# Performance work log

Hardware: AMD Instinct MI355X
Metric: run time of the kernel (lower is better)

Reference implementation:

```python
import jax, jax.numpy as jnp
import numpy as np

N_NODES = 100000
N_EDGES = 1200000
D = 64


def setup_inputs() -> dict:
    key = jax.random.key(0)
    ks = jax.random.split(key, 11)
    feats = jax.random.normal(ks[0], (N_NODES, D), dtype=jnp.float32)
    src = jax.random.randint(ks[1], (N_EDGES,), 0, N_NODES)
    dst = jax.random.randint(ks[2], (N_EDGES,), 0, N_NODES)
    s = 0.1  # small init scale
    W1 = jax.random.normal(ks[3], (D, D), dtype=jnp.float32) * s
    b1 = jnp.zeros((D,), dtype=jnp.float32)
    Wr1 = jax.random.normal(ks[4], (D, D), dtype=jnp.float32) * s
    br1 = jnp.zeros((D,), dtype=jnp.float32)
    W2 = jax.random.normal(ks[5], (D, D), dtype=jnp.float32) * s
    b2 = jnp.zeros((D,), dtype=jnp.float32)
    Wr2 = jax.random.normal(ks[6], (D, D), dtype=jnp.float32) * s
    br2 = jnp.zeros((D,), dtype=jnp.float32)
    return {"feats": feats, "W1": W1, "b1": b1, "Wr1": Wr1, "br1": br1,
            "W2": W2, "b2": b2, "Wr2": Wr2, "br2": br2,
            "src": src, "dst": dst}


def _gcn_layer(x, W, b, Wr, br, src, dst):
    # dgl GraphConv(norm='none'): aggregate sum of transformed neighbor feats + bias, then ReLU
    xw = x @ W                                        # [N, D]
    agg = jax.ops.segment_sum(xw[src], dst, num_segments=x.shape[0])  # gather-scatter
    conv = jax.nn.relu(agg + b)
    # residual branch: activation(Linear(feats))
    res = jax.nn.relu(x @ Wr + br)
    return conv + res  # dropout=0.0, batchnorm=False


def reference(feats, W1, b1, Wr1, br1, W2, b2, Wr2, br2, src, dst):
    h = _gcn_layer(feats, W1, b1, Wr1, br1, src, dst)
    h = _gcn_layer(h, W2, b2, Wr2, br2, src, dst)
    return h
```

## Files before the change

### kernel.cpp

```cpp
#include <hip/hip_runtime.h>

#define D 64
#define NBMAX 256
#define BCHUNK 4096
#define CAP 8192
#define CAP_PACK 12288

typedef unsigned short ushort_t;
typedef __attribute__((ext_vector_type(8))) short bf16x8;
typedef __attribute__((ext_vector_type(4))) float floatx4;

static __device__ __forceinline__ ushort_t f2bf(float x) {
  unsigned u = __float_as_uint(x);
  unsigned r = (u + 0x7FFF + ((u >> 16) & 1)) >> 16;
  return (ushort_t)r;
}
static __device__ __forceinline__ float bf2f(ushort_t u) {
  return __uint_as_float(((unsigned)u) << 16);
}

__global__ __launch_bounds__(256) void gemm_res_mfma_kernel(
    const float* __restrict__ x, const float* __restrict__ W,
    const float* __restrict__ Wr, const float* __restrict__ br,
    ushort_t* __restrict__ xw, ushort_t* __restrict__ res, int n_nodes,
    int* __restrict__ gtail, int* __restrict__ off_tail, int n_edges) {
  if (blockIdx.x == 0) {
    if (threadIdx.x < NBMAX) gtail[threadIdx.x] = (int)threadIdx.x * CAP_PACK;
    if (threadIdx.x == 0) *off_tail = n_edges;
  }
  const int lane = threadIdx.x & 63;
  const int wid = threadIdx.x >> 6;
  const int sub = lane & 15;
  const int q = lane >> 4;

  bf16x8 bW[4][2], bR[4][2];
#pragma unroll
  for (int t = 0; t < 4; ++t) {
#pragma unroll
    for (int s = 0; s < 2; ++s) {
      bf16x8 fw, fr;
#pragma unroll
      for (int j = 0; j < 8; ++j) {
        const int k = s * 32 + q * 8 + j;
        const int c = t * 16 + sub;
        fw[j] = (short)f2bf(W[k * D + c]);
        fr[j] = (short)f2bf(Wr[k * D + c]);
      }
      bW[t][s] = fw;
      bR[t][s] = fr;
    }
  }
  float brv[4];
#pragma unroll
  for (int t = 0; t < 4; ++t) brv[t] = br[t * 16 + sub];

  const int n_tiles = (n_nodes + 15) >> 4;
  const int wave_id = blockIdx.x * 4 + wid;
  const int n_waves = gridDim.x * 4;
  for (int tile = wave_id; tile < n_tiles; tile += n_waves) {
    const int n0 = tile << 4;
    const bool full = (n0 + 16 <= n_nodes);
    bf16x8 a0h, a0l, a1h, a1l;
    float v[16];
    if (full) {
      const float* xp = x + (size_t)(n0 + sub) * D + q * 8;
      *(float4*)(v + 0)  = *(const float4*)(xp);
      *(float4*)(v + 4)  = *(const float4*)(xp + 4);
      *(float4*)(v + 8)  = *(const float4*)(xp + 32);
      *(float4*)(v + 12) = *(const float4*)(xp + 36);
    } else {
      const bool ok = (n0 + sub) < n_nodes;
      const float* xp = x + (size_t)(n0 + sub) * D + q * 8;
#pragma unroll
      for (int j = 0; j < 8; ++j) {
        v[j] = ok ? xp[j] : 0.f;
        v[8 + j] = ok ? xp[32 + j] : 0.f;
      }
    }
#pragma unroll
    for (int j = 0; j < 8; ++j) {
      const ushort_t h0 = f2bf(v[j]);
      a0h[j] = (short)h0;
      a0l[j] = (short)f2bf(v[j] - bf2f(h0));
      const ushort_t h1 = f2bf(v[8 + j]);
      a1h[j] = (short)h1;
      a1l[j] = (short)f2bf(v[8 + j] - bf2f(h1));
    }
    floatx4 accW[4], accR[4];
#pragma unroll
    for (int t = 0; t < 4; ++t) {
      accW[t] = (floatx4){0.f, 0.f, 0.f, 0.f};
      accR[t] = (floatx4){0.f, 0.f, 0.f, 0.f};
    }
#pragma unroll
    for (int t = 0; t < 4; ++t) {
      accW[t] = __builtin_amdgcn_mfma_f32_16x16x32_bf16(a0h, bW[t][0], accW[t], 0, 0, 0);
      accW[t] = __builtin_amdgcn_mfma_f32_16x16x32_bf16(a0l, bW[t][0], accW[t], 0, 0, 0);
      accW[t] = __builtin_amdgcn_mfma_f32_16x16x32_bf16(a1h, bW[t][1], accW[t], 0, 0, 0);
      accW[t] = __builtin_amdgcn_mfma_f32_16x16x32_bf16(a1l, bW[t][1], accW[t], 0, 0, 0);
      accR[t] = __builtin_amdgcn_mfma_f32_16x16x32_bf16(a0h, bR[t][0], accR[t], 0, 0, 0);
      accR[t] = __builtin_amdgcn_mfma_f32_16x16x32_bf16(a0l, bR[t][0], accR[t], 0, 0, 0);
      accR[t] = __builtin_amdgcn_mfma_f32_16x16x32_bf16(a1h, bR[t][1], accR[t], 0, 0, 0);
      accR[t] = __builtin_amdgcn_mfma_f32_16x16x32_bf16(a1l, bR[t][1], accR[t], 0, 0, 0);
    }
    if (full) {
#pragma unroll
      for (int t = 0; t < 4; ++t) {
#pragma unroll
        for (int i = 0; i < 4; ++i) {
          const size_t r = (size_t)(n0 + q * 4 + i) * D + t * 16 + sub;
          xw[r] = f2bf(accW[t][i]);
          res[r] = f2bf(fmaxf(accR[t][i] + brv[t], 0.f));
        }
      }
    } else {
#pragma unroll
      for (int t = 0; t < 4; ++t) {
#pragma unroll
        for (int i = 0; i < 4; ++i) {
          const int rr = n0 + q * 4 + i;
          if (rr < n_nodes) {
            const size_t r = (size_t)rr * D + t * 16 + sub;
            xw[r] = f2bf(accW[t][i]);
            res[r] = f2bf(fmaxf(accR[t][i] + brv[t], 0.f));
          }
        }
      }
    }
  }
}

__global__ __launch_bounds__(256) void binpack_kernel(
    const int* __restrict__ src, const int* __restrict__ dst,
    int* __restrict__ gtail, unsigned* __restrict__ packed, int n_edges) {
  __shared__ int start[NBMAX], cur[NBMAX], gpos[NBMAX];
  __shared__ unsigned sorted[BCHUNK];
  __shared__ unsigned char bktid[BCHUNK];
  const int t = threadIdx.x;
  const int nchunk = (n_edges + BCHUNK - 1) / BCHUNK;
  for (int c = blockIdx.x; c < nchunk; c += gridDim.x) {
    cur[t] = 0;
    __syncthreads();
    const int e0 = c * BCHUNK;
    const int m = min(BCHUNK, n_edges - e0);
    int bk[16];
    unsigned pk[16];
#pragma unroll
    for (int k = 0; k < 16; ++k) {
      const int e = e0 + k * 256 + t;
      if (e < n_edges) {
        const int d = dst[e];
        const int s = src[e];
        bk[k] = d >> 9;
        pk[k] = ((unsigned)(d & 511) << 23) | (unsigned)s;
        atomicAdd(&cur[bk[k]], 1);
      } else {
        bk[k] = -1;
      }
    }
    __syncthreads();
    const int h = cur[t];
    start[t] = h;
    __syncthreads();
    for (int off = 1; off < NBMAX; off <<= 1) {
      const int v = (t >= off) ? start[t - off] : 0;
      __syncthreads();
      start[t] += v;
      __syncthreads();
    }
    const int excl = start[t] - h;
    __syncthreads();
    start[t] = excl;
    cur[t] = excl;
    __syncthreads();
#pragma unroll
    for (int k = 0; k < 16; ++k) {
      if (bk[k] >= 0) {
        const int pos = atomicAdd(&cur[bk[k]], 1);
        sorted[pos] = pk[k];
        bktid[pos] = (unsigned char)bk[k];
      }
    }
    __syncthreads();
    if (h > 0) gpos[t] = atomicAdd(&gtail[t], h);
    __syncthreads();
    for (int j = t; j < m; j += 256) {
      const int b = bktid[j];
      packed[gpos[b] + j - start[b]] = sorted[j];
    }
    __syncthreads();
  }
}

__global__ __launch_bounds__(256) void bucket_csr_kernel(
    const unsigned* __restrict__ packed, const int* __restrict__ gtail,
    int* __restrict__ csr_off, int* __restrict__ csr_src, int n_nodes,
    int nbuckets) {
  __shared__ int scnt[NBMAX], sexc[NBMAX];
  __shared__ int sc[2][512];
  __shared__ int cur[512];
  __shared__ unsigned outbuf[CAP];
  const int b = blockIdx.x;
  const int t = threadIdx.x;
  const int cb = (t < nbuckets) ? (gtail[t] - t * CAP_PACK) : 0;
  scnt[t] = cb;
  sexc[t] = cb;
  __syncthreads();
  for (int off = 1; off < NBMAX; off <<= 1) {
    const int v = (t >= off) ? sexc[t - off] : 0;
    __syncthreads();
    sexc[t] += v;
    __syncthreads();
  }
  sexc[t] -= scnt[t];
  __syncthreads();
  const int base = sexc[b];
  const int cntE = scnt[b];
  const unsigned* pk = packed + (size_t)b * CAP_PACK;

  const int n0 = b << 9;
  const int nn = min(512, n_nodes - n0);
  cur[t] = 0;
  cur[t + 256] = 0;
  __syncthreads();
  for (int i = t; i < cntE; i += 256) atomicAdd(&cur[pk[i] >> 23], 1);
  __syncthreads();
  const int h0 = cur[t];
  const int h1 = cur[t + 256];
  sc[0][t] = h0;
  sc[0][t + 256] = h1;
  __syncthreads();
  int pin = 0;
  for (int off = 1; off < 512; off <<= 1) {
    sc[1 - pin][t] = sc[pin][t] + ((t >= off) ? sc[pin][t - off] : 0);
    sc[1 - pin][t + 256] =
        sc[pin][t + 256] + ((t + 256 >= off) ? sc[pin][t + 256 - off] : 0);
    __syncthreads();
    pin ^= 1;
  }
  const int excl0 = sc[pin][t] - h0;
  const int excl1 = sc[pin][t + 256] - h1;
  if (t < nn) csr_off[n0 + t] = base + excl0;
  if (t + 256 < nn) csr_off[n0 + t + 256] = base + excl1;
  cur[t] = excl0;
  cur[t + 256] = excl1;
  __syncthreads();
  if (cntE <= CAP) {
    for (int i = t; i < cntE; i += 256) {
      const unsigned u = pk[i];
      const int pos = atomicAdd(&cur[u >> 23], 1);
      outbuf[pos] = u & 0x7FFFFFu;
    }
    __syncthreads();
    for (int j = t; j < cntE; j += 256) csr_src[base + j] = (int)outbuf[j];
  } else {
    for (int i = t; i < cntE; i += 256) {
      const unsigned u = pk[i];
      const int pos = atomicAdd(&cur[u >> 23], 1);
      csr_src[base + pos] = (int)(u & 0x7FFFFFu);
    }
  }
}

__global__ __launch_bounds__(256) void gather_gemm_kernel(
    const ushort_t* __restrict__ xw1, const ushort_t* __restrict__ res1,
    const float* __restrict__ b1v, const int* __restrict__ csr_off,
    const int* __restrict__ csr_src, const float* __restrict__ W2,
    const float* __restrict__ Wr2, const float* __restrict__ br2,
    ushort_t* __restrict__ xw2, ushort_t* __restrict__ res2, int n_nodes) {
  const int lane = threadIdx.x & 63;
  const int w = threadIdx.x >> 6;
  const int sub = lane & 15;
  const int q = lane >> 4;
  __shared__ float h_tile[16][68];

  bf16x8 bW[2], bR[2];
#pragma unroll
  for (int s = 0; s < 2; ++s) {
    bf16x8 fw, fr;
#pragma unroll
    for (int j = 0; j < 8; ++j) {
      const int k = s * 32 + q * 8 + j;
      const int c = w * 16 + sub;
      fw[j] = (short)f2bf(W2[k * D + c]);
      fr[j] = (short)f2bf(Wr2[k * D + c]);
    }
    bW[s] = fw;
    bR[s] = fr;
  }
  const float brl2 = br2[w * 16 + sub];
  const float4 bvec = *(const float4*)(b1v + sub * 4);

  const int n_tiles = (n_nodes + 15) >> 4;
  for (int tile = blockIdx.x; tile < n_tiles; tile += gridDim.x) {
    const int n0 = tile << 4;
    for (int j4 = 0; j4 < 4; ++j4) {
      const int n = n0 + w * 4 + j4;
      if (n < n_nodes) {
        const int e0 = csr_off[n];
        const int e1 = csr_off[n + 1];
        float4 acc = make_float4(0.f, 0.f, 0.f, 0.f);
        for (int base_e = e0; base_e < e1; base_e += 64) {
          const int m = min(64, e1 - base_e);
          const int idxv = (base_e + lane < e1) ? csr_src[base_e + lane] : 0;
          for (int j = 0; j < m; j += 4) {
            const int idx = __shfl(idxv, j + q, 64);
            if (j + q < m) {
              const ushort4 vv =
                  *(const ushort4*)(xw1 + ((size_t)idx << 6) + (sub << 2));
              acc.x += bf2f(vv.x);
              acc.y += bf2f(vv.y);
              acc.z += bf2f(vv.z);
              acc.w += bf2f(vv.w);
            }
          }
        }
#pragma unroll
        for (int mask = 32; mask >= 16; mask >>= 1) {
          acc.x += __shfl_xor(acc.x, mask, 64);
          acc.y += __shfl_xor(acc.y, mask, 64);
          acc.z += __shfl_xor(acc.z, mask, 64);
          acc.w += __shfl_xor(acc.w, mask, 64);
        }
        if (q == 0) {
          const ushort4 r =
              *(const ushort4*)(res1 + ((size_t)n << 6) + (sub << 2));
          float4 o;
          o.x = fmaxf(acc.x + bvec.x, 0.f) + bf2f(r.x);
          o.y = fmaxf(acc.y + bvec.y, 0.f) + bf2f(r.y);
          o.z = fmaxf(acc.z + bvec.z, 0.f) + bf2f(r.z);
          o.w = fmaxf(acc.w + bvec.w, 0.f) + bf2f(r.w);
          *(float4*)(&h_tile[w * 4 + j4][sub * 4]) = o;
        }
      } else if (q == 0) {
        *(float4*)(&h_tile[w * 4 + j4][sub * 4]) =
            make_float4(0.f, 0.f, 0.f, 0.f);
      }
    }
    __syncthreads();
    float v[16];
    *(float4*)(v + 0)  = *(const float4*)(&h_tile[sub][q * 8]);
    *(float4*)(v + 4)  = *(const float4*)(&h_tile[sub][q * 8 + 4]);
    *(float4*)(v + 8)  = *(const float4*)(&h_tile[sub][32 + q * 8]);
    *(float4*)(v + 12) = *(const float4*)(&h_tile[sub][32 + q * 8 + 4]);
    bf16x8 a0h, a0l, a1h, a1l;
#pragma unroll
    for (int j = 0; j < 8; ++j) {
      const ushort_t h0 = f2bf(v[j]);
      a0h[j] = (short)h0;
      a0l[j] = (short)f2bf(v[j] - bf2f(h0));
      const ushort_t h1 = f2bf(v[8 + j]);
      a1h[j] = (short)h1;
      a1l[j] = (short)f2bf(v[8 + j] - bf2f(h1));
    }
    floatx4 accW = (floatx4){0.f, 0.f, 0.f, 0.f};
    floatx4 accR = (floatx4){0.f, 0.f, 0.f, 0.f};
    accW = __builtin_amdgcn_mfma_f32_16x16x32_bf16(a0h, bW[0], accW, 0, 0, 0);
    accW = __builtin_amdgcn_mfma_f32_16x16x32_bf16(a0l, bW[0], accW, 0, 0, 0);
    accW = __builtin_amdgcn_mfma_f32_16x16x32_bf16(a1h, bW[1], accW, 0, 0, 0);
    accW = __builtin_amdgcn_mfma_f32_16x16x32_bf16(a1l, bW[1], accW, 0, 0, 0);
    accR = __builtin_amdgcn_mfma_f32_16x16x32_bf16(a0h, bR[0], accR, 0, 0, 0);
    accR = __builtin_amdgcn_mfma_f32_16x16x32_bf16(a0l, bR[0], accR, 0, 0, 0);
    accR = __builtin_amdgcn_mfma_f32_16x16x32_bf16(a1h, bR[1], accR, 0, 0, 0);
    accR = __builtin_amdgcn_mfma_f32_16x16x32_bf16(a1l, bR[1], accR, 0, 0, 0);
#pragma unroll
    for (int i = 0; i < 4; ++i) {
      const int rr = n0 + q * 4 + i;
      if (rr < n_nodes) {
        const size_t r = (size_t)rr * D + w * 16 + sub;
        xw2[r] = f2bf(accW[i]);
        res2[r] = f2bf(fmaxf(accR[i] + brl2, 0.f));
      }
    }
    __syncthreads();
  }
}

__global__ __launch_bounds__(256) void gather_combine_kernel(
    const ushort_t* __restrict__ xw, const ushort_t* __restrict__ res,
    const float* __restrict__ b, const int* __restrict__ csr_off,
    const int* __restrict__ csr_src, float* __restrict__ out, int n_nodes) {
  const int lane = threadIdx.x & 63;
  const int wid = threadIdx.x >> 6;
  const int grp = lane >> 4;
  const int sub = lane & 15;
  const float4 bvec = *(const float4*)(b + sub * 4);
  const int n_tiles = (n_nodes + 3) >> 2;
  for (int tile = blockIdx.x; tile < n_tiles; tile += gridDim.x) {
    const int n = tile * 4 + wid;
    if (n >= n_nodes) continue;
    const int e0 = csr_off[n];
    const int e1 = csr_off[n + 1];
    float4 acc = make_float4(0.f, 0.f, 0.f, 0.f);
    for (int base_e = e0; base_e < e1; base_e += 64) {
      const int m = min(64, e1 - base_e);
      const int idxv = (base_e + lane < e1) ? csr_src[base_e + lane] : 0;
      for (int j = 0; j < m; j += 4) {
        const int idx = __shfl(idxv, j + grp, 64);
        if (j + grp < m) {
          const ushort4 v =
              *(const ushort4*)(xw + ((size_t)idx << 6) + (sub << 2));
          acc.x += bf2f(v.x);
          acc.y += bf2f(v.y);
          acc.z += bf2f(v.z);
          acc.w += bf2f(v.w);
        }
      }
    }
#pragma unroll
    for (int mask = 32; mask >= 16; mask >>= 1) {
      acc.x += __shfl_xor(acc.x, mask, 64);
      acc.y += __shfl_xor(acc.y, mask, 64);
      acc.z += __shfl_xor(acc.z, mask, 64);
      acc.w += __shfl_xor(acc.w, mask, 64);
    }
    if (grp == 0) {
      const ushort4 r =
          *(const ushort4*)(res + ((size_t)n << 6) + (sub << 2));
      float4 o;
      o.x = fmaxf(acc.x + bvec.x, 0.f) + bf2f(r.x);
      o.y = fmaxf(acc.y + bvec.y, 0.f) + bf2f(r.y);
      o.z = fmaxf(acc.z + bvec.z, 0.f) + bf2f(r.z);
      o.w = fmaxf(acc.w + bvec.w, 0.f) + bf2f(r.w);
      *(float4*)(out + ((size_t)n << 6) + (sub << 2)) = o;
    }
  }
}

extern "C" void kernel_launch(void* const* d_in, const int* in_sizes, int n_in,
                              void* d_out, int out_size, void* d_ws, size_t ws_size,
                              hipStream_t stream) {
  const float* feats = (const float*)d_in[0];
  const float* W1  = (const float*)d_in[1];
  const float* b1  = (const float*)d_in[2];
  const float* Wr1 = (const float*)d_in[3];
  const float* br1 = (const float*)d_in[4];
  const float* W2  = (const float*)d_in[5];
  const float* b2  = (const float*)d_in[6];
  const float* Wr2 = (const float*)d_in[7];
  const float* br2 = (const float*)d_in[8];
  const int* src = (const int*)d_in[9];
  const int* dst = (const int*)d_in[10];
  const int n_nodes = in_sizes[0] / D;
  const int n_edges = in_sizes[9];
  float* out = (float*)d_out;

  const int nbuckets = (n_nodes + 511) >> 9;

  ushort_t* xw1 = (ushort_t*)d_ws;
  ushort_t* res1 = xw1 + (size_t)n_nodes * D;
  ushort_t* xw2 = res1 + (size_t)n_nodes * D;
  ushort_t* res2 = xw2 + (size_t)n_nodes * D;
  int* csr_off = (int*)(res2 + (size_t)n_nodes * D);
  int* csr_src = csr_off + (n_nodes + 1);
  int* gtail = csr_src + n_edges;
  unsigned* packed = (unsigned*)(gtail + NBMAX);

  const int tiles4 = (n_nodes + 3) / 4;
  const int gblocks = tiles4 < 2048 ? tiles4 : 2048;
  const int tiles16 = (n_nodes + 15) / 16;
  const int fblocks = tiles16 < 2048 ? tiles16 : 2048;
  const int nchunk = (n_edges + BCHUNK - 1) / BCHUNK;
  const int pblocks = nchunk < 1024 ? nchunk : 1024;
  dim3 blk(256);

  gemm_res_mfma_kernel<<<1024, blk, 0, stream>>>(
      feats, W1, Wr1, br1, xw1, res1, n_nodes, gtail, csr_off + n_nodes, n_edges);
  binpack_kernel<<<pblocks, blk, 0, stream>>>(src, dst, gtail, packed, n_edges);
  bucket_csr_kernel<<<nbuckets, blk, 0, stream>>>(packed, gtail, csr_off,
                                                  csr_src, n_nodes, nbuckets);
  gather_gemm_kernel<<<fblocks, blk, 0, stream>>>(
      xw1, res1, b1, csr_off, csr_src, W2, Wr2, br2, xw2, res2, n_nodes);
  gather_combine_kernel<<<gblocks, blk, 0, stream>>>(
      xw2, res2, b2, csr_off, csr_src, out, n_nodes);
}
```

Before: 253.9 us.

## Gather eight nodes per wave with 16-byte loads and unrolled neighbor prefetch

Both gather kernels now assign one node to each 8-lane group, so a wave handles eight nodes at once and each lane loads 16 bytes (8 bf16) per neighbor row. Before, a whole wave worked on one node with 4-lane-row splits and a cross-group shuffle reduction. The new code preloads up to 32 neighbor indices per node and runs a double-buffered, unrolled load/accumulate chain to keep more loads in flight, then falls back to a scalar loop past 32 edges. The gather_gemm tile grows to 32 nodes and runs two MFMA passes per tile. The risk is lane divergence when degrees within a group of eight nodes differ, plus higher register pressure.

```diff
diff --git a/kernel.cpp b/kernel.cpp
--- a/kernel.cpp
+++ b/kernel.cpp
@@ -17,6 +17,97 @@
 }
 static __device__ __forceinline__ float bf2f(ushort_t u) {
   return __uint_as_float(((unsigned)u) << 16);
+}
+
+static __device__ __forceinline__ void addrow(const uint4 v, float2& a0,
+                                              float2& a1, float2& a2,
+                                              float2& a3) {
+  a0.x += __uint_as_float(v.x << 16);
+  a0.y += __uint_as_float(v.x & 0xffff0000u);
+  a1.x += __uint_as_float(v.y << 16);
+  a1.y += __uint_as_float(v.y & 0xffff0000u);
+  a2.x += __uint_as_float(v.z << 16);
+  a2.y += __uint_as_float(v.z & 0xffff0000u);
+  a3.x += __uint_as_float(v.w << 16);
+  a3.y += __uint_as_float(v.w & 0xffff0000u);
+}
+
+#define GLOAD4(T0, T1, T2, T3, IR, OFF, CB)                                    \
+  do {                                                                         \
+    const int s0_ = __shfl((IR), gbase + (OFF) + 0, 64);                       \
+    const int s1_ = __shfl((IR), gbase + (OFF) + 1, 64);                       \
+    const int s2_ = __shfl((IR), gbase + (OFF) + 2, 64);                       \
+    const int s3_ = __shfl((IR), gbase + (OFF) + 3, 64);                       \
+    T0 = ((CB) + 0 < m) ? *(const uint4*)(tab + ((size_t)s0_ << 6) + off16)    \
+                        : z4;                                                  \
+    T1 = ((CB) + 1 < m) ? *(const uint4*)(tab + ((size_t)s1_ << 6) + off16)    \
+                        : z4;                                                  \
+    T2 = ((CB) + 2 < m) ? *(const uint4*)(tab + ((size_t)s2_ << 6) + off16)    \
+                        : z4;                                                  \
+    T3 = ((CB) + 3 < m) ? *(const uint4*)(tab + ((size_t)s3_ << 6) + off16)    \
+                        : z4;                                                  \
+  } while (0)
+
+#define ACC4(T0, T1, T2, T3)    \
+  do {                          \
+    addrow(T0, c0, c1, c2, c3); \
+    addrow(T1, c0, c1, c2, c3); \
+    addrow(T2, c0, c1, c2, c3); \
+    addrow(T3, c0, c1, c2, c3); \
+  } while (0)
+
+static __device__ __forceinline__ void gather_node8(
+    const ushort_t* __restrict__ tab, const int* __restrict__ csr_src, int e0,
+    int e1, int sub8, int gbase, float2& c0, float2& c1, float2& c2,
+    float2& c3) {
+  const int off16 = sub8 << 3;
+  const int m = e1 - e0;
+  const int ir0 = (e0 + 0 + sub8 < e1) ? csr_src[e0 + 0 + sub8] : 0;
+  const int ir1 = (e0 + 8 + sub8 < e1) ? csr_src[e0 + 8 + sub8] : 0;
+  const int ir2 = (e0 + 16 + sub8 < e1) ? csr_src[e0 + 16 + sub8] : 0;
+  const int ir3 = (e0 + 24 + sub8 < e1) ? csr_src[e0 + 24 + sub8] : 0;
+  int mm = m;
+  mm = max(mm, __shfl_xor(mm, 8, 64));
+  mm = max(mm, __shfl_xor(mm, 16, 64));
+  mm = max(mm, __shfl_xor(mm, 32, 64));
+  const int nch = __builtin_amdgcn_readfirstlane(min((mm + 3) >> 2, 8));
+  const uint4 z4 = make_uint4(0, 0, 0, 0);
+  uint4 A0, A1, A2, A3, B0, B1, B2, B3;
+  if (nch > 0) {
+    GLOAD4(A0, A1, A2, A3, ir0, 0, 0);
+    if (nch > 1) GLOAD4(B0, B1, B2, B3, ir0, 4, 4);
+    ACC4(A0, A1, A2, A3);
+    if (nch > 1) {
+      if (nch > 2) GLOAD4(A0, A1, A2, A3, ir1, 0, 8);
+      ACC4(B0, B1, B2, B3);
+      if (nch > 2) {
+        if (nch > 3) GLOAD4(B0, B1, B2, B3, ir1, 4, 12);
+        ACC4(A0, A1, A2, A3);
+        if (nch > 3) {
+          if (nch > 4) GLOAD4(A0, A1, A2, A3, ir2, 0, 16);
+          ACC4(B0, B1, B2, B3);
+          if (nch > 4) {
+            if (nch > 5) GLOAD4(B0, B1, B2, B3, ir2, 4, 20);
+            ACC4(A0, A1, A2, A3);
+            if (nch > 5) {
+              if (nch > 6) GLOAD4(A0, A1, A2, A3, ir3, 0, 24);
+              ACC4(B0, B1, B2, B3);
+              if (nch > 6) {
+                if (nch > 7) GLOAD4(B0, B1, B2, B3, ir3, 4, 28);
+                ACC4(A0, A1, A2, A3);
+                if (nch > 7) ACC4(B0, B1, B2, B3);
+              }
+            }
+          }
+        }
+      }
+    }
+  }
+  for (int eb = e0 + 32; eb < e1; ++eb) {
+    const int ii = csr_src[eb];
+    const uint4 tv = *(const uint4*)(tab + ((size_t)ii << 6) + off16);
+    addrow(tv, c0, c1, c2, c3);
+  }
 }
 
 __global__ __launch_bounds__(256) void gemm_res_mfma_kernel(
@@ -272,7 +363,10 @@
   const int w = threadIdx.x >> 6;
   const int sub = lane & 15;
   const int q = lane >> 4;
-  __shared__ float h_tile[16][68];
+  const int sub8 = lane & 7;
+  const int g = lane >> 3;
+  const int gbase = lane & 56;
+  __shared__ float h_tile[32][68];
 
   bf16x8 bW[2], bR[2];
 #pragma unroll
@@ -289,87 +383,75 @@
     bR[s] = fr;
   }
   const float brl2 = br2[w * 16 + sub];
-  const float4 bvec = *(const float4*)(b1v + sub * 4);
-
-  const int n_tiles = (n_nodes + 15) >> 4;
+  const float2 bz0 = *(const float2*)(b1v + sub8 * 8 + 0);
+  const float2 bz1 = *(const float2*)(b1v + sub8 * 8 + 2);
+  const float2 bz2 = *(const float2*)(b1v + sub8 * 8 + 4);
+  const float2 bz3 = *(const float2*)(b1v + sub8 * 8 + 6);
+
+  const int n_tiles = (n_nodes + 31) >> 5;
   for (int tile = blockIdx.x; tile < n_tiles; tile += gridDim.x) {
-    const int n0 = tile << 4;
-    for (int j4 = 0; j4 < 4; ++j4) {
-      const int n = n0 + w * 4 + j4;
-      if (n < n_nodes) {
-        const int e0 = csr_off[n];
-        const int e1 = csr_off[n + 1];
-        float4 acc = make_float4(0.f, 0.f, 0.f, 0.f);
-        for (int base_e = e0; base_e < e1; base_e += 64) {
-          const int m = min(64, e1 - base_e);
-          const int idxv = (base_e + lane < e1) ? csr_src[base_e + lane] : 0;
-          for (int j = 0; j < m; j += 4) {
-            const int idx = __shfl(idxv, j + q, 64);
-            if (j + q < m) {
-              const ushort4 vv =
-                  *(const ushort4*)(xw1 + ((size_t)idx << 6) + (sub << 2));
-              acc.x += bf2f(vv.x);
-              acc.y += bf2f(vv.y);
-              acc.z += bf2f(vv.z);
-              acc.w += bf2f(vv.w);
-            }
-          }
+    const int n0 = tile << 5;
+    const int nb = n0 + w * 8;
+    const int offv = csr_off[min(nb + (lane < 9 ? lane : 8), n_nodes)];
+    const int e0 = __shfl(offv, g, 64);
+    const int e1 = __shfl(offv, g + 1, 64);
+    float2 c0 = {0.f, 0.f}, c1 = {0.f, 0.f}, c2 = {0.f, 0.f}, c3 = {0.f, 0.f};
+    gather_node8(xw1, csr_src, e0, e1, sub8, gbase, c0, c1, c2, c3);
+    const int n = nb + g;
+    const int row = (w << 3) + g;
+    if (n < n_nodes) {
+      const uint4 rv = *(const uint4*)(res1 + ((size_t)n << 6) + (sub8 << 3));
+      float4 lo, hi;
+      lo.x = fmaxf(c0.x + bz0.x, 0.f) + __uint_as_float(rv.x << 16);
+      lo.y = fmaxf(c0.y + bz0.y, 0.f) + __uint_as_float(rv.x & 0xffff0000u);
+      lo.z = fmaxf(c1.x + bz1.x, 0.f) + __uint_as_float(rv.y << 16);
+      lo.w = fmaxf(c1.y + bz1.y, 0.f) + __uint_as_float(rv.y & 0xffff0000u);
+      hi.x = fmaxf(c2.x + bz2.x, 0.f) + __uint_as_float(rv.z << 16);
+      hi.y = fmaxf(c2.y + bz2.y, 0.f) + __uint_as_float(rv.z & 0xffff0000u);
+      hi.z = fmaxf(c3.x + bz3.x, 0.f) + __uint_as_float(rv.w << 16);
+      hi.w = fmaxf(c3.y + bz3.y, 0.f) + __uint_as_float(rv.w & 0xffff0000u);
+      *(float4*)(&h_tile[row][sub8 * 8]) = lo;
+      *(float4*)(&h_tile[row][sub8 * 8 + 4]) = hi;
+    } else {
+      *(float4*)(&h_tile[row][sub8 * 8]) = make_float4(0.f, 0.f, 0.f, 0.f);
+      *(float4*)(&h_tile[row][sub8 * 8 + 4]) = make_float4(0.f, 0.f, 0.f, 0.f);
+    }
+    __syncthreads();
+#pragma unroll
+    for (int st = 0; st < 2; ++st) {
+      float v[16];
+      *(float4*)(v + 0)  = *(const float4*)(&h_tile[st * 16 + sub][q * 8]);
+      *(float4*)(v + 4)  = *(const float4*)(&h_tile[st * 16 + sub][q * 8 + 4]);
+      *(float4*)(v + 8)  = *(const float4*)(&h_tile[st * 16 + sub][32 + q * 8]);
+      *(float4*)(v + 12) = *(const float4*)(&h_tile[st * 16 + sub][32 + q * 8 + 4]);
+      bf16x8 a0h, a0l, a1h, a1l;
+#pragma unroll
+      for (int j = 0; j < 8; ++j) {
+        const ushort_t h0 = f2bf(v[j]);
+        a0h[j] = (short)h0;
+        a0l[j] = (short)f2bf(v[j] - bf2f(h0));
+        const ushort_t h1 = f2bf(v[8 + j]);
+        a1h[j] = (short)h1;
+        a1l[j] = (short)f2bf(v[8 + j] - bf2f(h1));
+      }
+      floatx4 accW = (floatx4){0.f, 0.f, 0.f, 0.f};
+      floatx4 accR = (floatx4){0.f, 0.f, 0.f, 0.f};
+      accW = __builtin_amdgcn_mfma_f32_16x16x32_bf16(a0h, bW[0], accW, 0, 0, 0);
+      accW = __builtin_amdgcn_mfma_f32_16x16x32_bf16(a0l, bW[0], accW, 0, 0, 0);
+      accW = __builtin_amdgcn_mfma_f32_16x16x32_bf16(a1h, bW[1], accW, 0, 0, 0);
+      accW = __builtin_amdgcn_mfma_f32_16x16x32_bf16(a1l, bW[1], accW, 0, 0, 0);
+      accR = __builtin_amdgcn_mfma_f32_16x16x32_bf16(a0h, bR[0], accR, 0, 0, 0);
+      accR = __builtin_amdgcn_mfma_f32_16x16x32_bf16(a0l, bR[0], accR, 0, 0, 0);
+      accR = __builtin_amdgcn_mfma_f32_16x16x32_bf16(a1h, bR[1], accR, 0, 0, 0);
+      accR = __builtin_amdgcn_mfma_f32_16x16x32_bf16(a1l, bR[1], accR, 0, 0, 0);
+#pragma unroll
+      for (int i = 0; i < 4; ++i) {
+        const int rr = n0 + st * 16 + q * 4 + i;
+        if (rr < n_nodes) {
+          const size_t r = (size_t)rr * D + w * 16 + sub;
+          xw2[r] = f2bf(accW[i]);
+          res2[r] = f2bf(fmaxf(accR[i] + brl2, 0.f));
         }
-#pragma unroll
-        for (int mask = 32; mask >= 16; mask >>= 1) {
-          acc.x += __shfl_xor(acc.x, mask, 64);
-          acc.y += __shfl_xor(acc.y, mask, 64);
-          acc.z += __shfl_xor(acc.z, mask, 64);
-          acc.w += __shfl_xor(acc.w, mask, 64);
-        }
-        if (q == 0) {
-          const ushort4 r =
-              *(const ushort4*)(res1 + ((size_t)n << 6) + (sub << 2));
-          float4 o;
-          o.x = fmaxf(acc.x + bvec.x, 0.f) + bf2f(r.x);
-          o.y = fmaxf(acc.y + bvec.y, 0.f) + bf2f(r.y);
-          o.z = fmaxf(acc.z + bvec.z, 0.f) + bf2f(r.z);
-          o.w = fmaxf(acc.w + bvec.w, 0.f) + bf2f(r.w);
-          *(float4*)(&h_tile[w * 4 + j4][sub * 4]) = o;
-        }
-      } else if (q == 0) {
-        *(float4*)(&h_tile[w * 4 + j4][sub * 4]) =
-            make_float4(0.f, 0.f, 0.f, 0.f);
-      }
-    }
-    __syncthreads();
-    float v[16];
-    *(float4*)(v + 0)  = *(const float4*)(&h_tile[sub][q * 8]);
-    *(float4*)(v + 4)  = *(const float4*)(&h_tile[sub][q * 8 + 4]);
-    *(float4*)(v + 8)  = *(const float4*)(&h_tile[sub][32 + q * 8]);
-    *(float4*)(v + 12) = *(const float4*)(&h_tile[sub][32 + q * 8 + 4]);
-    bf16x8 a0h, a0l, a1h, a1l;
-#pragma unroll
-    for (int j = 0; j < 8; ++j) {
-      const ushort_t h0 = f2bf(v[j]);
-      a0h[j] = (short)h0;
-      a0l[j] = (short)f2bf(v[j] - bf2f(h0));
-      const ushort_t h1 = f2bf(v[8 + j]);
-      a1h[j] = (short)h1;
-      a1l[j] = (short)f2bf(v[8 + j] - bf2f(h1));
-    }
-    floatx4 accW = (floatx4){0.f, 0.f, 0.f, 0.f};
-    floatx4 accR = (floatx4){0.f, 0.f, 0.f, 0.f};
-    accW = __builtin_amdgcn_mfma_f32_16x16x32_bf16(a0h, bW[0], accW, 0, 0, 0);
-    accW = __builtin_amdgcn_mfma_f32_16x16x32_bf16(a0l, bW[0], accW, 0, 0, 0);
-    accW = __builtin_amdgcn_mfma_f32_16x16x32_bf16(a1h, bW[1], accW, 0, 0, 0);
-    accW = __builtin_amdgcn_mfma_f32_16x16x32_bf16(a1l, bW[1], accW, 0, 0, 0);
-    accR = __builtin_amdgcn_mfma_f32_16x16x32_bf16(a0h, bR[0], accR, 0, 0, 0);
-    accR = __builtin_amdgcn_mfma_f32_16x16x32_bf16(a0l, bR[0], accR, 0, 0, 0);
-    accR = __builtin_amdgcn_mfma_f32_16x16x32_bf16(a1h, bR[1], accR, 0, 0, 0);
-    accR = __builtin_amdgcn_mfma_f32_16x16x32_bf16(a1l, bR[1], accR, 0, 0, 0);
-#pragma unroll
-    for (int i = 0; i < 4; ++i) {
-      const int rr = n0 + q * 4 + i;
-      if (rr < n_nodes) {
-        const size_t r = (size_t)rr * D + w * 16 + sub;
-        xw2[r] = f2bf(accW[i]);
-        res2[r] = f2bf(fmaxf(accR[i] + brl2, 0.f));
       }
     }
     __syncthreads();
@@ -381,48 +463,36 @@
     const float* __restrict__ b, const int* __restrict__ csr_off,
     const int* __restrict__ csr_src, float* __restrict__ out, int n_nodes) {
   const int lane = threadIdx.x & 63;
-  const int wid = threadIdx.x >> 6;
-  const int grp = lane >> 4;
-  const int sub = lane & 15;
-  const float4 bvec = *(const float4*)(b + sub * 4);
-  const int n_tiles = (n_nodes + 3) >> 2;
+  const int w = threadIdx.x >> 6;
+  const int sub8 = lane & 7;
+  const int g = lane >> 3;
+  const int gbase = lane & 56;
+  const float2 bz0 = *(const float2*)(b + sub8 * 8 + 0);
+  const float2 bz1 = *(const float2*)(b + sub8 * 8 + 2);
+  const float2 bz2 = *(const float2*)(b + sub8 * 8 + 4);
+  const float2 bz3 = *(const float2*)(b + sub8 * 8 + 6);
+  const int n_tiles = (n_nodes + 31) >> 5;
   for (int tile = blockIdx.x; tile < n_tiles; tile += gridDim.x) {
-    const int n = tile * 4 + wid;
-    if (n >= n_nodes) continue;
-    const int e0 = csr_off[n];
-    const int e1 = csr_off[n + 1];
-    float4 acc = make_float4(0.f, 0.f, 0.f, 0.f);
-    for (int base_e = e0; base_e < e1; base_e += 64) {
-      const int m = min(64, e1 - base_e);
-      const int idxv = (base_e + lane < e1) ? csr_src[base_e + lane] : 0;
-      for (int j = 0; j < m; j += 4) {
-        const int idx = __shfl(idxv, j + grp, 64);
-        if (j + grp < m) {
-          const ushort4 v =
-              *(const ushort4*)(xw + ((size_t)idx << 6) + (sub << 2));
-          acc.x += bf2f(v.x);
-          acc.y += bf2f(v.y);
-          acc.z += bf2f(v.z);
-          acc.w += bf2f(v.w);
-        }
-      }
-    }
-#pragma unroll
-    for (int mask = 32; mask >= 16; mask >>= 1) {
-      acc.x += __shfl_xor(acc.x, mask, 64);
-      acc.y += __shfl_xor(acc.y, mask, 64);
-      acc.z += __shfl_xor(acc.z, mask, 64);
-      acc.w += __shfl_xor(acc.w, mask, 64);
-    }
-    if (grp == 0) {
-      const ushort4 r =
-          *(const ushort4*)(res + ((size_t)n << 6) + (sub << 2));
-      float4 o;
-      o.x = fmaxf(acc.x + bvec.x, 0.f) + bf2f(r.x);
-      o.y = fmaxf(acc.y + bvec.y, 0.f) + bf2f(r.y);
-      o.z = fmaxf(acc.z + bvec.z, 0.f) + bf2f(r.z);
-      o.w = fmaxf(acc.w + bvec.w, 0.f) + bf2f(r.w);
-      *(float4*)(out + ((size_t)n << 6) + (sub << 2)) = o;
+    const int nb = (tile << 5) + w * 8;
+    const int offv = csr_off[min(nb + (lane < 9 ? lane : 8), n_nodes)];
+    const int e0 = __shfl(offv, g, 64);
+    const int e1 = __shfl(offv, g + 1, 64);
+    float2 c0 = {0.f, 0.f}, c1 = {0.f, 0.f}, c2 = {0.f, 0.f}, c3 = {0.f, 0.f};
+    gather_node8(xw, csr_src, e0, e1, sub8, gbase, c0, c1, c2, c3);
+    const int n = nb + g;
+    if (n < n_nodes) {
+      const uint4 rv = *(const uint4*)(res + ((size_t)n << 6) + (sub8 << 3));
+      float4 lo, hi;
+      lo.x = fmaxf(c0.x + bz0.x, 0.f) + __uint_as_float(rv.x << 16);
+      lo.y = fmaxf(c0.y + bz0.y, 0.f) + __uint_as_float(rv.x & 0xffff0000u);
+      lo.z = fmaxf(c1.x + bz1.x, 0.f) + __uint_as_float(rv.y << 16);
+      lo.w = fmaxf(c1.y + bz1.y, 0.f) + __uint_as_float(rv.y & 0xffff0000u);
+      hi.x = fmaxf(c2.x + bz2.x, 0.f) + __uint_as_float(rv.z << 16);
+      hi.y = fmaxf(c2.y + bz2.y, 0.f) + __uint_as_float(rv.z & 0xffff0000u);
+      hi.z = fmaxf(c3.x + bz3.x, 0.f) + __uint_as_float(rv.w << 16);
+      hi.w = fmaxf(c3.y + bz3.y, 0.f) + __uint_as_float(rv.w & 0xffff0000u);
+      *(float4*)(out + ((size_t)n << 6) + sub8 * 8) = lo;
+      *(float4*)(out + ((size_t)n << 6) + sub8 * 8 + 4) = hi;
     }
   }
 }
@@ -456,10 +526,9 @@
   int* gtail = csr_src + n_edges;
   unsigned* packed = (unsigned*)(gtail + NBMAX);
 
-  const int tiles4 = (n_nodes + 3) / 4;
-  const int gblocks = tiles4 < 2048 ? tiles4 : 2048;
-  const int tiles16 = (n_nodes + 15) / 16;
-  const int fblocks = tiles16 < 2048 ? tiles16 : 2048;
+  const int tiles32 = (n_nodes + 31) / 32;
+  const int gblocks = tiles32 < 2048 ? tiles32 : 2048;
+  const int fblocks = tiles32 < 2048 ? tiles32 : 2048;
   const int nchunk = (n_edges + BCHUNK - 1) / BCHUNK;
   const int pblocks = nchunk < 1024 ? nchunk : 1024;
   dim3 blk(256);
```

After: 229.9 us. 9.5% less time.
